# Performance work log

Measured on AMD Instinct MI355X. Metric: run time of the kernel, lower is better.

The kernel has to match this reference:

```python
import jax, jax.numpy as jnp
import numpy as np

NUM_GROUPS = 17
NUM_OCCLUDED = 10
TEMP = 0.1


def setup_inputs() -> dict:
    key = jax.random.key(0)
    k1, k2 = jax.random.split(key)
    B, N, D = 128, 577, 768
    x = jax.random.normal(k1, (B, N, D), dtype=jnp.float32)
    # xavier_uniform-like scale for (D, G) weight
    bound = float(np.sqrt(6.0 / (D + NUM_GROUPS)))
    group_weights = jax.random.uniform(k2, (D, NUM_GROUPS), dtype=jnp.float32, minval=-bound, maxval=bound)
    return {"x": x, "group_weights": group_weights}


def _l2_normalize(v):
    # matches F.normalize(dim=-1, eps=1e-12)
    return v / jnp.maximum(jnp.linalg.norm(v, axis=-1, keepdims=True), 1e-12)


def reference(x, group_weights):
    B, N, D = x.shape
    cls_token = x[:, 0, :]            # (B, D)
    patch_tokens = x[:, 1:, :]        # (B, P, D), P = N-1

    # cosine similarity of each patch with cls token
    sim = jnp.einsum('bpd,bd->bp', _l2_normalize(patch_tokens), _l2_normalize(cls_token))  # (B, P)

    # k least-similar patches are "occluded" -> zero them out
    _, occ_idx = jax.lax.top_k(-sim, NUM_OCCLUDED)  # (B, K)
    mask = jnp.ones_like(sim).at[jnp.arange(B)[:, None], occ_idx].set(0.0)  # (B, P)
    non_occ = patch_tokens * mask[..., None]  # (B, P, D)

    # attention-style group pooling; softmax over groups (dim=1)
    scores = jnp.einsum('dg,bpd->bgp', group_weights, non_occ) / TEMP  # (B, G, P)
    attn = jax.nn.softmax(scores, axis=1)
    group_features = jnp.einsum('bgp,bpd->bgd', attn, non_occ)  # (B, G, D)

    # pack [global_feat, group_feat_1..G] as (B, 1+G, D)
    feats = jnp.concatenate([cls_token[:, None, :], group_features], axis=1)
    return feats, attn
```

## Files before the change

kernel.cpp:

```cpp
#include <hip/hip_runtime.h>
#include <math.h>

#define B_ 128
#define NTOK 577
#define P_ 576
#define D_ 768
#define G_ 17
#define KOCC 10
#define INV_TEMP 10.0f
#define U17 (1.0f / 17.0f)

#define OFF_WT 0
#define OFF_SIM (G_ * D_)
#define OFF_CLSINV (OFF_SIM + B_ * P_)
#define OFF_OCC (OFF_CLSINV + B_)
#define OFF_GFP (OFF_OCC + B_ * KOCC)
#define GFP_PART ((size_t)B_ * G_ * D_)

__global__ __launch_bounds__(256) void k0_cls(const float* __restrict__ x,
                                              const float* __restrict__ gw,
                                              float* __restrict__ feats,
                                              float* __restrict__ clsinv,
                                              float* __restrict__ wt,
                                              int zero_groups) {
    if (blockIdx.x >= B_) {
        int g = blockIdx.x - B_;
        for (int d = threadIdx.x; d < D_; d += 256)
            wt[g * D_ + d] = gw[d * G_ + g];
        return;
    }
    int b = blockIdx.x;
    const float* cls = x + (size_t)b * NTOK * D_;
    float* fb = feats + (size_t)b * 18 * D_;
    float ss = 0.f;
    for (int i = threadIdx.x; i < D_ / 4; i += 256) {
        float4 v = ((const float4*)cls)[i];
        ((float4*)fb)[i] = v;
        ss = fmaf(v.x, v.x, fmaf(v.y, v.y, fmaf(v.z, v.z, fmaf(v.w, v.w, ss))));
    }
    if (zero_groups) {
        float4 z = {0.f, 0.f, 0.f, 0.f};
        for (int i = threadIdx.x; i < G_ * D_ / 4; i += 256)
            ((float4*)(fb + D_))[i] = z;
    }
    #pragma unroll
    for (int off = 32; off; off >>= 1) ss += __shfl_xor(ss, off, 64);
    __shared__ float red[4];
    int wave = threadIdx.x >> 6, lane = threadIdx.x & 63;
    if (lane == 0) red[wave] = ss;
    __syncthreads();
    if (threadIdx.x == 0) {
        float t = red[0] + red[1] + red[2] + red[3];
        clsinv[b] = 1.0f / fmaxf(sqrtf(t), 1e-12f);
    }
}

__global__ __launch_bounds__(256) void k1_score(const float* __restrict__ x,
                                                const float* __restrict__ wt,
                                                const float* __restrict__ clsinv,
                                                float* __restrict__ sim,
                                                float* __restrict__ attn) {
    __shared__ __align__(16) float buf[2][18 * 64];
    __shared__ __align__(16) float atile[19 * 68];
    int tid = threadIdx.x;
    int b = blockIdx.y, chunk = blockIdx.x;
    const float* clsrow = x + (size_t)b * NTOK * D_;

    for (int i = tid; i < 288; i += 256) {
        int r = i >> 4, c = i & 15;
        const float* src = (r < 17) ? (wt + r * D_ + c * 4) : (clsrow + c * 4);
        *(float4*)&buf[0][r * 64 + c * 4] = *(const float4*)src;
    }
    int lane = tid & 63, wave = tid >> 6;
    int lr = lane & 15, row4 = lane >> 4;
    int pbase = wave * 16 + row4 * 4;
    const float* xp0 = x + ((size_t)(b * NTOK + 1 + chunk * 64 + pbase)) * D_ + lr * 4;

    float4 xv[4], xn[4];
    #pragma unroll
    for (int m = 0; m < 4; ++m) xv[m] = *(const float4*)(xp0 + (size_t)m * D_);

    float s[19][4];
    #pragma unroll
    for (int i = 0; i < 19; ++i)
        #pragma unroll
        for (int m = 0; m < 4; ++m) s[i][m] = 0.f;
    __syncthreads();

    for (int kc = 0; kc < 12; ++kc) {
        int cb = kc & 1, nb = cb ^ 1;
        if (kc < 11) {
            #pragma unroll
            for (int m = 0; m < 4; ++m)
                xn[m] = *(const float4*)(xp0 + (kc + 1) * 64 + (size_t)m * D_);
            for (int i = tid; i < 288; i += 256) {
                int r = i >> 4, c = i & 15;
                const float* src = (r < 17) ? (wt + r * D_ + (kc + 1) * 64 + c * 4)
                                            : (clsrow + (kc + 1) * 64 + c * 4);
                *(float4*)&buf[nb][r * 64 + c * 4] = *(const float4*)src;
            }
        }
        #pragma unroll
        for (int g = 0; g < 18; ++g) {
            float4 w4 = *(const float4*)&buf[cb][g * 64 + lr * 4];
            #pragma unroll
            for (int m = 0; m < 4; ++m)
                s[g][m] = fmaf(xv[m].x, w4.x, fmaf(xv[m].y, w4.y,
                          fmaf(xv[m].z, w4.z, fmaf(xv[m].w, w4.w, s[g][m]))));
        }
        #pragma unroll
        for (int m = 0; m < 4; ++m)
            s[18][m] = fmaf(xv[m].x, xv[m].x, fmaf(xv[m].y, xv[m].y,
                       fmaf(xv[m].z, xv[m].z, fmaf(xv[m].w, xv[m].w, s[18][m]))));
        #pragma unroll
        for (int m = 0; m < 4; ++m) xv[m] = xn[m];
        __syncthreads();
    }

    #pragma unroll
    for (int off = 8; off >= 1; off >>= 1)
        #pragma unroll
        for (int i = 0; i < 19; ++i)
            #pragma unroll
            for (int m = 0; m < 4; ++m)
                s[i][m] += __shfl_xor(s[i][m], off, 16);

    #pragma unroll
    for (int g = 0; g < 19; ++g) {
        if (lr == ((g < 16) ? g : 15)) {
            float4 v = {s[g][0], s[g][1], s[g][2], s[g][3]};
            *(float4*)&atile[g * 68 + pbase] = v;
        }
    }
    __syncthreads();

    if (tid < 64) {
        int p = chunk * 64 + tid;
        float v[17];
        float mx = -3.0e38f;
        #pragma unroll
        for (int g = 0; g < 17; ++g) {
            v[g] = atile[g * 68 + tid];
            mx = fmaxf(mx, v[g]);
        }
        float tot = 0.f;
        #pragma unroll
        for (int g = 0; g < 17; ++g) {
            v[g] = __expf((v[g] - mx) * INV_TEMP);
            tot += v[g];
        }
        float inv = 1.0f / tot;
        float* ap = attn + ((size_t)b * G_) * P_ + p;
        #pragma unroll
        for (int g = 0; g < 17; ++g) ap[(size_t)g * P_] = v[g] * inv;
        float cd = atile[17 * 68 + tid];
        float sq = atile[18 * 68 + tid];
        sim[(size_t)b * P_ + p] = cd * clsinv[b] / fmaxf(sqrtf(sq), 1e-12f);
    }
}

__global__ __launch_bounds__(64) void k2_occl(const float* __restrict__ sim,
                                              float* __restrict__ attn,
                                              int* __restrict__ occ_idx) {
    int b = blockIdx.x, lane = threadIdx.x;
    int base = lane * 9;
    float v[9];
    #pragma unroll
    for (int j = 0; j < 9; ++j) v[j] = sim[(size_t)b * P_ + base + j];
    int wins[KOCC];
    for (int t = 0; t < KOCC; ++t) {
        float mv = 3.0e38f;
        int mi = 1 << 30;
        #pragma unroll
        for (int j = 0; j < 9; ++j) {
            if (v[j] < mv) { mv = v[j]; mi = base + j; }
        }
        #pragma unroll
        for (int off = 1; off < 64; off <<= 1) {
            float ov = __shfl_xor(mv, off, 64);
            int oi = __shfl_xor(mi, off, 64);
            if (ov < mv || (ov == mv && oi < mi)) { mv = ov; mi = oi; }
        }
        wins[t] = mi;
        int loc = mi - base;
        if (loc >= 0 && loc < 9) v[loc] = 3.0e38f;
    }
    if (lane == 0) {
        #pragma unroll
        for (int t = 0; t < KOCC; ++t) occ_idx[b * KOCC + t] = wins[t];
    }
    #pragma unroll
    for (int t = 0; t < KOCC; ++t) {
        if (lane < G_) attn[((size_t)b * G_ + lane) * P_ + wins[t]] = U17;
    }
}

__global__ __launch_bounds__(192) void k3_part(const float* __restrict__ x,
                                               const float* __restrict__ attn,
                                               float* __restrict__ gfp,
                                               int ppp) {
    extern __shared__ float am[];
    int tid = threadIdx.x;
    int pc = blockIdx.x, b = blockIdx.y;
    int p0 = pc * ppp;

    for (int i = tid; i < G_ * ppp; i += 192) {
        int g = i / ppp;
        int pp = i - g * ppp;
        am[i] = attn[((size_t)b * G_ + g) * P_ + p0 + pp];
    }
    __syncthreads();

    const float* xb = x + ((size_t)(b * NTOK) + 1 + p0) * D_ + tid * 4;
    float4 acc[G_];
    #pragma unroll
    for (int g = 0; g < G_; ++g) acc[g] = make_float4(0.f, 0.f, 0.f, 0.f);

    float4 c0 = *(const float4*)(xb + (size_t)0 * D_);
    float4 c1 = *(const float4*)(xb + (size_t)1 * D_);
    float4 c2 = *(const float4*)(xb + (size_t)2 * D_);
    float4 c3 = *(const float4*)(xb + (size_t)3 * D_);

    for (int pp = 0; pp < ppp; pp += 4) {
        float4 n0, n1, n2, n3;
        if (pp + 4 < ppp) {
            n0 = *(const float4*)(xb + (size_t)(pp + 4) * D_);
            n1 = *(const float4*)(xb + (size_t)(pp + 5) * D_);
            n2 = *(const float4*)(xb + (size_t)(pp + 6) * D_);
            n3 = *(const float4*)(xb + (size_t)(pp + 7) * D_);
        }
        #pragma unroll
        for (int g = 0; g < G_; ++g) {
            float4 a = *(const float4*)&am[g * ppp + pp];
            acc[g].x = fmaf(a.x, c0.x, fmaf(a.y, c1.x, fmaf(a.z, c2.x, fmaf(a.w, c3.x, acc[g].x))));
            acc[g].y = fmaf(a.x, c0.y, fmaf(a.y, c1.y, fmaf(a.z, c2.y, fmaf(a.w, c3.y, acc[g].y))));
            acc[g].z = fmaf(a.x, c0.z, fmaf(a.y, c1.z, fmaf(a.z, c2.z, fmaf(a.w, c3.z, acc[g].z))));
            acc[g].w = fmaf(a.x, c0.w, fmaf(a.y, c1.w, fmaf(a.z, c2.w, fmaf(a.w, c3.w, acc[g].w))));
        }
        c0 = n0; c1 = n1; c2 = n2; c3 = n3;
    }

    float* gb = gfp + ((size_t)(pc * B_ + b) * G_) * D_ + tid * 4;
    #pragma unroll
    for (int g = 0; g < G_; ++g) *(float4*)(gb + (size_t)g * D_) = acc[g];
}

#define PC_ 96
__global__ __launch_bounds__(192) void k3_atomic(const float* __restrict__ x,
                                                 const float* __restrict__ attn,
                                                 float* __restrict__ feats) {
    __shared__ __align__(16) float am[G_ * PC_];
    int tid = threadIdx.x;
    int pc = blockIdx.x, b = blockIdx.y;
    int p0 = pc * PC_;
    for (int i = tid; i < G_ * PC_; i += 192) {
        int g = i / PC_;
        int pp = i - g * PC_;
        am[i] = attn[((size_t)b * G_ + g) * P_ + p0 + pp];
    }
    __syncthreads();
    const float* xb = x + ((size_t)(b * NTOK) + 1 + p0) * D_ + tid * 4;
    float4 acc[G_];
    #pragma unroll
    for (int g = 0; g < G_; ++g) acc[g] = make_float4(0.f, 0.f, 0.f, 0.f);
    for (int pp = 0; pp < PC_; pp += 4) {
        float4 x0 = *(const float4*)(xb + (size_t)(pp + 0) * D_);
        float4 x1 = *(const float4*)(xb + (size_t)(pp + 1) * D_);
        float4 x2 = *(const float4*)(xb + (size_t)(pp + 2) * D_);
        float4 x3 = *(const float4*)(xb + (size_t)(pp + 3) * D_);
        #pragma unroll
        for (int g = 0; g < G_; ++g) {
            float4 a = *(const float4*)&am[g * PC_ + pp];
            acc[g].x = fmaf(a.x, x0.x, fmaf(a.y, x1.x, fmaf(a.z, x2.x, fmaf(a.w, x3.x, acc[g].x))));
            acc[g].y = fmaf(a.x, x0.y, fmaf(a.y, x1.y, fmaf(a.z, x2.y, fmaf(a.w, x3.y, acc[g].y))));
            acc[g].z = fmaf(a.x, x0.z, fmaf(a.y, x1.z, fmaf(a.z, x2.z, fmaf(a.w, x3.z, acc[g].z))));
            acc[g].w = fmaf(a.x, x0.w, fmaf(a.y, x1.w, fmaf(a.z, x2.w, fmaf(a.w, x3.w, acc[g].w))));
        }
    }
    float* fb = feats + ((size_t)(b * 18) + 1) * D_ + tid * 4;
    #pragma unroll
    for (int g = 0; g < G_; ++g) {
        atomicAdd(fb + (size_t)g * D_ + 0, acc[g].x);
        atomicAdd(fb + (size_t)g * D_ + 1, acc[g].y);
        atomicAdd(fb + (size_t)g * D_ + 2, acc[g].z);
        atomicAdd(fb + (size_t)g * D_ + 3, acc[g].w);
    }
}

__global__ __launch_bounds__(192) void k4_fin(const float* __restrict__ x,
                                              const int* __restrict__ occ_idx,
                                              const float* __restrict__ gfp,
                                              int nparts,
                                              float* __restrict__ feats) {
    int b = blockIdx.x, tid = threadIdx.x;
    float* fb = feats + ((size_t)(b * 18) + 1) * D_ + tid * 4;
    float4 acc[G_];
    if (nparts == 0) {
        #pragma unroll
        for (int g = 0; g < G_; ++g) acc[g] = *(const float4*)(fb + (size_t)g * D_);
    } else {
        #pragma unroll
        for (int g = 0; g < G_; ++g) acc[g] = make_float4(0.f, 0.f, 0.f, 0.f);
        for (int pc = 0; pc < nparts; ++pc) {
            const float* gb = gfp + ((size_t)(pc * B_ + b) * G_) * D_ + tid * 4;
            #pragma unroll
            for (int g = 0; g < G_; ++g) {
                float4 v = *(const float4*)(gb + (size_t)g * D_);
                acc[g].x += v.x; acc[g].y += v.y; acc[g].z += v.z; acc[g].w += v.w;
            }
        }
    }
    float4 corr = make_float4(0.f, 0.f, 0.f, 0.f);
    for (int t = 0; t < KOCC; ++t) {
        int p = occ_idx[b * KOCC + t];
        float4 xo = *(const float4*)(x + ((size_t)(b * NTOK) + 1 + p) * D_ + tid * 4);
        corr.x += xo.x; corr.y += xo.y; corr.z += xo.z; corr.w += xo.w;
    }
    corr.x *= U17; corr.y *= U17; corr.z *= U17; corr.w *= U17;
    #pragma unroll
    for (int g = 0; g < G_; ++g) {
        float4 v = acc[g];
        v.x -= corr.x; v.y -= corr.y; v.z -= corr.z; v.w -= corr.w;
        *(float4*)(fb + (size_t)g * D_) = v;
    }
}

extern "C" void kernel_launch(void* const* d_in, const int* in_sizes, int n_in,
                              void* d_out, int out_size, void* d_ws, size_t ws_size,
                              hipStream_t stream) {
    const float* x  = (const float*)d_in[0];
    const float* gw = (const float*)d_in[1];
    float* feats = (float*)d_out;
    float* attn  = (float*)d_out + (size_t)B_ * 18 * D_;
    float* wt      = (float*)d_ws + OFF_WT;
    float* sim     = (float*)d_ws + OFF_SIM;
    float* clsinv  = (float*)d_ws + OFF_CLSINV;
    int*   occ_idx = (int*)((float*)d_ws + OFF_OCC);
    float* gfp     = (float*)d_ws + OFF_GFP;

    int nparts = 0;
    for (int n = 4; n >= 1; n >>= 1) {
        if ((OFF_GFP + (size_t)n * GFP_PART) * 4 <= ws_size) { nparts = n; break; }
    }

    k0_cls<<<B_ + G_, 256, 0, stream>>>(x, gw, feats, clsinv, wt, nparts == 0);
    k1_score<<<dim3(9, B_), 256, 0, stream>>>(x, wt, clsinv, sim, attn);
    k2_occl<<<B_, 64, 0, stream>>>(sim, attn, occ_idx);
    if (nparts > 0) {
        int ppp = P_ / nparts;
        k3_part<<<dim3(nparts, B_), 192, G_ * ppp * 4, stream>>>(x, attn, gfp, ppp);
    } else {
        k3_atomic<<<dim3(P_ / PC_, B_), 192, 0, stream>>>(x, attn, feats);
    }
    k4_fin<<<B_, 192, 0, stream>>>(x, occ_idx, gfp, nparts, feats);
}
```

Measured before the change: 413.2 us.

## Fuse group pooling into score kernel and correct occluded patches afterwards

The scoring kernel now also performs the attention-weighted group pooling on its 64-patch chunk while the data is hot, writing per-chunk partials (or atomics when workspace is short). Occlusion is handled afterwards: the finalize kernel subtracts each occluded patch's contribution using its original softmax weight, and patches attn to 1/17. This removes the separate second pass over x for pooling, at the cost of more partial slabs to reduce (9 instead of up to 4) and a larger workspace requirement. The cls norm scaling is dropped since it does not change the ranking of similarities.

```diff
diff --git a/kernel.cpp b/kernel.cpp
--- a/kernel.cpp
+++ b/kernel.cpp
@@ -9,57 +9,34 @@
 #define KOCC 10
 #define INV_TEMP 10.0f
 #define U17 (1.0f / 17.0f)
+#define NPART 9
 
 #define OFF_WT 0
 #define OFF_SIM (G_ * D_)
-#define OFF_CLSINV (OFF_SIM + B_ * P_)
-#define OFF_OCC (OFF_CLSINV + B_)
+#define OFF_OCC (OFF_SIM + B_ * P_)
 #define OFF_GFP (OFF_OCC + B_ * KOCC)
-#define GFP_PART ((size_t)B_ * G_ * D_)
-
-__global__ __launch_bounds__(256) void k0_cls(const float* __restrict__ x,
-                                              const float* __restrict__ gw,
-                                              float* __restrict__ feats,
-                                              float* __restrict__ clsinv,
-                                              float* __restrict__ wt,
-                                              int zero_groups) {
-    if (blockIdx.x >= B_) {
-        int g = blockIdx.x - B_;
-        for (int d = threadIdx.x; d < D_; d += 256)
-            wt[g * D_ + d] = gw[d * G_ + g];
-        return;
-    }
+#define GFP_SLAB ((size_t)B_ * G_ * D_)
+
+__global__ __launch_bounds__(256) void k0_wt(const float* __restrict__ gw,
+                                             float* __restrict__ wt) {
+    int g = blockIdx.x;
+    for (int d = threadIdx.x; d < D_; d += 256)
+        wt[g * D_ + d] = gw[d * G_ + g];
+}
+
+__global__ __launch_bounds__(256) void k0_zero(float* __restrict__ feats) {
     int b = blockIdx.x;
-    const float* cls = x + (size_t)b * NTOK * D_;
-    float* fb = feats + (size_t)b * 18 * D_;
-    float ss = 0.f;
-    for (int i = threadIdx.x; i < D_ / 4; i += 256) {
-        float4 v = ((const float4*)cls)[i];
-        ((float4*)fb)[i] = v;
-        ss = fmaf(v.x, v.x, fmaf(v.y, v.y, fmaf(v.z, v.z, fmaf(v.w, v.w, ss))));
-    }
-    if (zero_groups) {
-        float4 z = {0.f, 0.f, 0.f, 0.f};
-        for (int i = threadIdx.x; i < G_ * D_ / 4; i += 256)
-            ((float4*)(fb + D_))[i] = z;
-    }
-    #pragma unroll
-    for (int off = 32; off; off >>= 1) ss += __shfl_xor(ss, off, 64);
-    __shared__ float red[4];
-    int wave = threadIdx.x >> 6, lane = threadIdx.x & 63;
-    if (lane == 0) red[wave] = ss;
-    __syncthreads();
-    if (threadIdx.x == 0) {
-        float t = red[0] + red[1] + red[2] + red[3];
-        clsinv[b] = 1.0f / fmaxf(sqrtf(t), 1e-12f);
-    }
-}
-
-__global__ __launch_bounds__(256) void k1_score(const float* __restrict__ x,
-                                                const float* __restrict__ wt,
-                                                const float* __restrict__ clsinv,
-                                                float* __restrict__ sim,
-                                                float* __restrict__ attn) {
+    float4 z = {0.f, 0.f, 0.f, 0.f};
+    float4* fb = (float4*)(feats + (size_t)b * 18 * D_ + D_);
+    for (int i = threadIdx.x; i < G_ * D_ / 4; i += 256) fb[i] = z;
+}
+
+__global__ __launch_bounds__(256) void k13_fused(const float* __restrict__ x,
+                                                 const float* __restrict__ wt,
+                                                 float* __restrict__ sim,
+                                                 float* __restrict__ attn,
+                                                 float* __restrict__ gfp,
+                                                 float* __restrict__ feats) {
     __shared__ __align__(16) float buf[2][18 * 64];
     __shared__ __align__(16) float atile[19 * 68];
     int tid = threadIdx.x;
@@ -152,22 +129,69 @@
         float inv = 1.0f / tot;
         float* ap = attn + ((size_t)b * G_) * P_ + p;
         #pragma unroll
-        for (int g = 0; g < 17; ++g) ap[(size_t)g * P_] = v[g] * inv;
+        for (int g = 0; g < 17; ++g) {
+            float a = v[g] * inv;
+            ap[(size_t)g * P_] = a;
+            atile[g * 68 + tid] = a;
+        }
         float cd = atile[17 * 68 + tid];
         float sq = atile[18 * 68 + tid];
-        sim[(size_t)b * P_ + p] = cd * clsinv[b] / fmaxf(sqrtf(sq), 1e-12f);
+        sim[(size_t)b * P_ + p] = cd / fmaxf(sqrtf(sq), 1e-12f);
+    }
+    __syncthreads();
+
+    if (tid < 192) {
+        const float* xb = x + ((size_t)(b * NTOK + 1 + chunk * 64)) * D_ + tid * 4;
+        float4 acc[G_];
+        #pragma unroll
+        for (int g = 0; g < G_; ++g) acc[g] = make_float4(0.f, 0.f, 0.f, 0.f);
+
+        float4 c0 = *(const float4*)(xb + (size_t)0 * D_);
+        float4 c1 = *(const float4*)(xb + (size_t)1 * D_);
+        float4 c2 = *(const float4*)(xb + (size_t)2 * D_);
+        float4 c3 = *(const float4*)(xb + (size_t)3 * D_);
+        for (int pp = 0; pp < 64; pp += 4) {
+            float4 n0, n1, n2, n3;
+            if (pp + 4 < 64) {
+                n0 = *(const float4*)(xb + (size_t)(pp + 4) * D_);
+                n1 = *(const float4*)(xb + (size_t)(pp + 5) * D_);
+                n2 = *(const float4*)(xb + (size_t)(pp + 6) * D_);
+                n3 = *(const float4*)(xb + (size_t)(pp + 7) * D_);
+            }
+            #pragma unroll
+            for (int g = 0; g < G_; ++g) {
+                float4 a = *(const float4*)&atile[g * 68 + pp];
+                acc[g].x = fmaf(a.x, c0.x, fmaf(a.y, c1.x, fmaf(a.z, c2.x, fmaf(a.w, c3.x, acc[g].x))));
+                acc[g].y = fmaf(a.x, c0.y, fmaf(a.y, c1.y, fmaf(a.z, c2.y, fmaf(a.w, c3.y, acc[g].y))));
+                acc[g].z = fmaf(a.x, c0.z, fmaf(a.y, c1.z, fmaf(a.z, c2.z, fmaf(a.w, c3.z, acc[g].z))));
+                acc[g].w = fmaf(a.x, c0.w, fmaf(a.y, c1.w, fmaf(a.z, c2.w, fmaf(a.w, c3.w, acc[g].w))));
+            }
+            c0 = n0; c1 = n1; c2 = n2; c3 = n3;
+        }
+        if (gfp) {
+            float* gb = gfp + ((size_t)(chunk * B_ + b) * G_) * D_ + tid * 4;
+            #pragma unroll
+            for (int g = 0; g < G_; ++g) *(float4*)(gb + (size_t)g * D_) = acc[g];
+        } else {
+            float* fb = feats + ((size_t)(b * 18) + 1) * D_ + tid * 4;
+            #pragma unroll
+            for (int g = 0; g < G_; ++g) {
+                atomicAdd(fb + (size_t)g * D_ + 0, acc[g].x);
+                atomicAdd(fb + (size_t)g * D_ + 1, acc[g].y);
+                atomicAdd(fb + (size_t)g * D_ + 2, acc[g].z);
+                atomicAdd(fb + (size_t)g * D_ + 3, acc[g].w);
+            }
+        }
     }
 }
 
 __global__ __launch_bounds__(64) void k2_occl(const float* __restrict__ sim,
-                                              float* __restrict__ attn,
                                               int* __restrict__ occ_idx) {
     int b = blockIdx.x, lane = threadIdx.x;
     int base = lane * 9;
     float v[9];
     #pragma unroll
     for (int j = 0; j < 9; ++j) v[j] = sim[(size_t)b * P_ + base + j];
-    int wins[KOCC];
     for (int t = 0; t < KOCC; ++t) {
         float mv = 3.0e38f;
         int mi = 1 << 30;
@@ -181,123 +205,39 @@
             int oi = __shfl_xor(mi, off, 64);
             if (ov < mv || (ov == mv && oi < mi)) { mv = ov; mi = oi; }
         }
-        wins[t] = mi;
+        if (lane == 0) occ_idx[b * KOCC + t] = mi;
         int loc = mi - base;
         if (loc >= 0 && loc < 9) v[loc] = 3.0e38f;
-    }
-    if (lane == 0) {
-        #pragma unroll
-        for (int t = 0; t < KOCC; ++t) occ_idx[b * KOCC + t] = wins[t];
-    }
-    #pragma unroll
-    for (int t = 0; t < KOCC; ++t) {
-        if (lane < G_) attn[((size_t)b * G_ + lane) * P_ + wins[t]] = U17;
-    }
-}
-
-__global__ __launch_bounds__(192) void k3_part(const float* __restrict__ x,
-                                               const float* __restrict__ attn,
-                                               float* __restrict__ gfp,
-                                               int ppp) {
-    extern __shared__ float am[];
-    int tid = threadIdx.x;
-    int pc = blockIdx.x, b = blockIdx.y;
-    int p0 = pc * ppp;
-
-    for (int i = tid; i < G_ * ppp; i += 192) {
-        int g = i / ppp;
-        int pp = i - g * ppp;
-        am[i] = attn[((size_t)b * G_ + g) * P_ + p0 + pp];
-    }
-    __syncthreads();
-
-    const float* xb = x + ((size_t)(b * NTOK) + 1 + p0) * D_ + tid * 4;
-    float4 acc[G_];
-    #pragma unroll
-    for (int g = 0; g < G_; ++g) acc[g] = make_float4(0.f, 0.f, 0.f, 0.f);
-
-    float4 c0 = *(const float4*)(xb + (size_t)0 * D_);
-    float4 c1 = *(const float4*)(xb + (size_t)1 * D_);
-    float4 c2 = *(const float4*)(xb + (size_t)2 * D_);
-    float4 c3 = *(const float4*)(xb + (size_t)3 * D_);
-
-    for (int pp = 0; pp < ppp; pp += 4) {
-        float4 n0, n1, n2, n3;
-        if (pp + 4 < ppp) {
-            n0 = *(const float4*)(xb + (size_t)(pp + 4) * D_);
-            n1 = *(const float4*)(xb + (size_t)(pp + 5) * D_);
-            n2 = *(const float4*)(xb + (size_t)(pp + 6) * D_);
-            n3 = *(const float4*)(xb + (size_t)(pp + 7) * D_);
-        }
-        #pragma unroll
-        for (int g = 0; g < G_; ++g) {
-            float4 a = *(const float4*)&am[g * ppp + pp];
-            acc[g].x = fmaf(a.x, c0.x, fmaf(a.y, c1.x, fmaf(a.z, c2.x, fmaf(a.w, c3.x, acc[g].x))));
-            acc[g].y = fmaf(a.x, c0.y, fmaf(a.y, c1.y, fmaf(a.z, c2.y, fmaf(a.w, c3.y, acc[g].y))));
-            acc[g].z = fmaf(a.x, c0.z, fmaf(a.y, c1.z, fmaf(a.z, c2.z, fmaf(a.w, c3.z, acc[g].z))));
-            acc[g].w = fmaf(a.x, c0.w, fmaf(a.y, c1.w, fmaf(a.z, c2.w, fmaf(a.w, c3.w, acc[g].w))));
-        }
-        c0 = n0; c1 = n1; c2 = n2; c3 = n3;
-    }
-
-    float* gb = gfp + ((size_t)(pc * B_ + b) * G_) * D_ + tid * 4;
-    #pragma unroll
-    for (int g = 0; g < G_; ++g) *(float4*)(gb + (size_t)g * D_) = acc[g];
-}
-
-#define PC_ 96
-__global__ __launch_bounds__(192) void k3_atomic(const float* __restrict__ x,
-                                                 const float* __restrict__ attn,
-                                                 float* __restrict__ feats) {
-    __shared__ __align__(16) float am[G_ * PC_];
-    int tid = threadIdx.x;
-    int pc = blockIdx.x, b = blockIdx.y;
-    int p0 = pc * PC_;
-    for (int i = tid; i < G_ * PC_; i += 192) {
-        int g = i / PC_;
-        int pp = i - g * PC_;
-        am[i] = attn[((size_t)b * G_ + g) * P_ + p0 + pp];
-    }
-    __syncthreads();
-    const float* xb = x + ((size_t)(b * NTOK) + 1 + p0) * D_ + tid * 4;
-    float4 acc[G_];
-    #pragma unroll
-    for (int g = 0; g < G_; ++g) acc[g] = make_float4(0.f, 0.f, 0.f, 0.f);
-    for (int pp = 0; pp < PC_; pp += 4) {
-        float4 x0 = *(const float4*)(xb + (size_t)(pp + 0) * D_);
-        float4 x1 = *(const float4*)(xb + (size_t)(pp + 1) * D_);
-        float4 x2 = *(const float4*)(xb + (size_t)(pp + 2) * D_);
-        float4 x3 = *(const float4*)(xb + (size_t)(pp + 3) * D_);
-        #pragma unroll
-        for (int g = 0; g < G_; ++g) {
-            float4 a = *(const float4*)&am[g * PC_ + pp];
-            acc[g].x = fmaf(a.x, x0.x, fmaf(a.y, x1.x, fmaf(a.z, x2.x, fmaf(a.w, x3.x, acc[g].x))));
-            acc[g].y = fmaf(a.x, x0.y, fmaf(a.y, x1.y, fmaf(a.z, x2.y, fmaf(a.w, x3.y, acc[g].y))));
-            acc[g].z = fmaf(a.x, x0.z, fmaf(a.y, x1.z, fmaf(a.z, x2.z, fmaf(a.w, x3.z, acc[g].z))));
-            acc[g].w = fmaf(a.x, x0.w, fmaf(a.y, x1.w, fmaf(a.z, x2.w, fmaf(a.w, x3.w, acc[g].w))));
-        }
-    }
-    float* fb = feats + ((size_t)(b * 18) + 1) * D_ + tid * 4;
-    #pragma unroll
-    for (int g = 0; g < G_; ++g) {
-        atomicAdd(fb + (size_t)g * D_ + 0, acc[g].x);
-        atomicAdd(fb + (size_t)g * D_ + 1, acc[g].y);
-        atomicAdd(fb + (size_t)g * D_ + 2, acc[g].z);
-        atomicAdd(fb + (size_t)g * D_ + 3, acc[g].w);
     }
 }
 
 __global__ __launch_bounds__(192) void k4_fin(const float* __restrict__ x,
                                               const int* __restrict__ occ_idx,
                                               const float* __restrict__ gfp,
-                                              int nparts,
-                                              float* __restrict__ feats) {
+                                              float* __restrict__ attn,
+                                              float* __restrict__ feats,
+                                              int nparts) {
+    __shared__ float ao[G_ * KOCC];
+    __shared__ int op[KOCC];
     int b = blockIdx.x, tid = threadIdx.x;
-    float* fb = feats + ((size_t)(b * 18) + 1) * D_ + tid * 4;
+    if (tid < KOCC) op[tid] = occ_idx[b * KOCC + tid];
+    __syncthreads();
+    if (tid < G_ * KOCC) {
+        int g = tid / KOCC, t = tid - g * KOCC;
+        float* ap = attn + ((size_t)b * G_ + g) * P_ + op[t];
+        ao[tid] = *ap;
+        *ap = U17;
+    }
+    __syncthreads();
+
+    float* fb = feats + (size_t)b * 18 * D_ + tid * 4;
+    *(float4*)fb = *(const float4*)(x + (size_t)b * NTOK * D_ + tid * 4);
+
     float4 acc[G_];
     if (nparts == 0) {
         #pragma unroll
-        for (int g = 0; g < G_; ++g) acc[g] = *(const float4*)(fb + (size_t)g * D_);
+        for (int g = 0; g < G_; ++g)
+            acc[g] = *(const float4*)(fb + (size_t)(1 + g) * D_);
     } else {
         #pragma unroll
         for (int g = 0; g < G_; ++g) acc[g] = make_float4(0.f, 0.f, 0.f, 0.f);
@@ -310,19 +250,20 @@
             }
         }
     }
-    float4 corr = make_float4(0.f, 0.f, 0.f, 0.f);
     for (int t = 0; t < KOCC; ++t) {
-        int p = occ_idx[b * KOCC + t];
-        float4 xo = *(const float4*)(x + ((size_t)(b * NTOK) + 1 + p) * D_ + tid * 4);
-        corr.x += xo.x; corr.y += xo.y; corr.z += xo.z; corr.w += xo.w;
-    }
-    corr.x *= U17; corr.y *= U17; corr.z *= U17; corr.w *= U17;
-    #pragma unroll
-    for (int g = 0; g < G_; ++g) {
-        float4 v = acc[g];
-        v.x -= corr.x; v.y -= corr.y; v.z -= corr.z; v.w -= corr.w;
-        *(float4*)(fb + (size_t)g * D_) = v;
-    }
+        float4 xo = *(const float4*)(x + ((size_t)(b * NTOK) + 1 + op[t]) * D_ + tid * 4);
+        #pragma unroll
+        for (int g = 0; g < G_; ++g) {
+            float a = ao[g * KOCC + t];
+            acc[g].x = fmaf(-a, xo.x, acc[g].x);
+            acc[g].y = fmaf(-a, xo.y, acc[g].y);
+            acc[g].z = fmaf(-a, xo.z, acc[g].z);
+            acc[g].w = fmaf(-a, xo.w, acc[g].w);
+        }
+    }
+    #pragma unroll
+    for (int g = 0; g < G_; ++g)
+        *(float4*)(fb + (size_t)(1 + g) * D_) = acc[g];
 }
 
 extern "C" void kernel_launch(void* const* d_in, const int* in_sizes, int n_in,
@@ -334,23 +275,16 @@
     float* attn  = (float*)d_out + (size_t)B_ * 18 * D_;
     float* wt      = (float*)d_ws + OFF_WT;
     float* sim     = (float*)d_ws + OFF_SIM;
-    float* clsinv  = (float*)d_ws + OFF_CLSINV;
     int*   occ_idx = (int*)((float*)d_ws + OFF_OCC);
     float* gfp     = (float*)d_ws + OFF_GFP;
 
-    int nparts = 0;
-    for (int n = 4; n >= 1; n >>= 1) {
-        if ((OFF_GFP + (size_t)n * GFP_PART) * 4 <= ws_size) { nparts = n; break; }
-    }
-
-    k0_cls<<<B_ + G_, 256, 0, stream>>>(x, gw, feats, clsinv, wt, nparts == 0);
-    k1_score<<<dim3(9, B_), 256, 0, stream>>>(x, wt, clsinv, sim, attn);
-    k2_occl<<<B_, 64, 0, stream>>>(sim, attn, occ_idx);
-    if (nparts > 0) {
-        int ppp = P_ / nparts;
-        k3_part<<<dim3(nparts, B_), 192, G_ * ppp * 4, stream>>>(x, attn, gfp, ppp);
-    } else {
-        k3_atomic<<<dim3(P_ / PC_, B_), 192, 0, stream>>>(x, attn, feats);
-    }
-    k4_fin<<<B_, 192, 0, stream>>>(x, occ_idx, gfp, nparts, feats);
-}
+    bool use_gfp = (OFF_GFP + (size_t)NPART * GFP_SLAB) * 4 <= ws_size;
+
+    k0_wt<<<G_, 256, 0, stream>>>(gw, wt);
+    if (!use_gfp) k0_zero<<<B_, 256, 0, stream>>>(feats);
+    k13_fused<<<dim3(NPART, B_), 256, 0, stream>>>(x, wt, sim, attn,
+                                                   use_gfp ? gfp : nullptr, feats);
+    k2_occl<<<B_, 64, 0, stream>>>(sim, occ_idx);
+    k4_fin<<<B_, 192, 0, stream>>>(x, occ_idx, gfp, attn, feats,
+                                   use_gfp ? NPART : 0);
+}
```

New measurement: 420.4 us. No clear change (+1.7%).
